# Kernel tuning notes

Hardware: AMD Instinct MI355X
Metric: run time of the kernel (lower is better)

## Reference

```python
import jax, jax.numpy as jnp
import numpy as np

N = 50000          # nodes
E = 800000         # edges
IN_C = 128
HID = 64
NUM_GRAPHS = 256
OUT_C = 8


def setup_inputs() -> dict:
    key = jax.random.key(0)
    k1, k2, k3, k4, k5, k6, k7 = jax.random.split(key, 7)
    x = jax.random.normal(k1, (N, IN_C), dtype=jnp.float32)
    edge_index = jax.random.randint(k2, (2, E), 0, N, dtype=jnp.int64)
    batch = jnp.sort(jax.random.randint(k3, (N,), 0, NUM_GRAPHS, dtype=jnp.int64))
    # GCNConv params (lin: in->hid, glorot-ish) and fc params (hid->8)
    W = jax.random.normal(k4, (IN_C, HID), dtype=jnp.float32) / np.sqrt(IN_C)
    b = jnp.zeros((HID,), dtype=jnp.float32)
    Wfc = jax.random.normal(k5, (HID, OUT_C), dtype=jnp.float32) / np.sqrt(HID)
    bfc = jnp.zeros((OUT_C,), dtype=jnp.float32)
    return {"x": x, "edge_index": edge_index, "batch": batch,
            "W": W, "b": b, "Wfc": Wfc, "bfc": bfc}


def reference(x, edge_index, batch, W, b, Wfc, bfc):
    n = x.shape[0]
    # GCNConv: linear transform first, then normalized propagation w/ self-loops
    x_lin = x @ W                                             # [N, HID]
    self_loops = jnp.arange(n, dtype=edge_index.dtype)
    row = jnp.concatenate([edge_index[0], self_loops])        # src
    col = jnp.concatenate([edge_index[1], self_loops])        # dst
    # symmetric normalization: deg over destinations (weight = 1)
    deg = jax.ops.segment_sum(jnp.ones_like(col, dtype=x.dtype), col,
                              num_segments=n)                 # [N]
    dinv = jnp.where(deg > 0, jax.lax.rsqrt(deg), 0.0)
    norm = dinv[row] * dinv[col]                              # [E+N]
    msg = x_lin[row] * norm[:, None]                          # gather + scale
    h = jax.ops.segment_sum(msg, col, num_segments=n) + b     # scatter-add
    h = jax.nn.relu(h)
    # global_mean_pool over batch ids
    sums = jax.ops.segment_sum(h, batch, num_segments=NUM_GRAPHS)
    cnts = jax.ops.segment_sum(jnp.ones((n,), dtype=x.dtype), batch,
                               num_segments=NUM_GRAPHS)
    pooled = sums / jnp.maximum(cnts, 1.0)[:, None]           # [G, HID]
    return pooled @ Wfc + bfc                                 # [G, 8]
```

## Files before the change

### kernel.cpp

```cpp
#include <hip/hip_runtime.h>
#include <stdint.h>

#define N_NODES 50000
#define N_EDGES 800000
#define IN_C    128
#define HID     64
#define NUM_G   256
#define OUT_C   8

#define NBH   64
#define ES    (N_EDGES / NBH)
#define NBIN  50048
#define NPK   (NBIN / 2)

#define NQ_H   4
#define BINS_H (NBIN / NQ_H)
#define PK_H   (BINS_H / 2)
#define NQ_S   4
#define BINS_S (NBIN / NQ_S)

#define NBLK_CSR   98
#define NBLK_LIN   512
#define NTILE      1563
#define NBLK_SCALE 200
#define NCHUNK     (N_NODES * 8)
#define GPOOL_GRID 782

__device__ __forceinline__ unsigned short f2bf(float f) {
    union { float f; unsigned u; } v; v.f = f;
    unsigned r = v.u + 0x7fff + ((v.u >> 16) & 1);
    return (unsigned short)(r >> 16);
}
__device__ __forceinline__ float4 bf4(uint2 u) {
    union { unsigned u; float f; } a, b, c, d;
    a.u = u.x << 16;  b.u = u.x & 0xffff0000u;
    c.u = u.y << 16;  d.u = u.y & 0xffff0000u;
    return make_float4(a.f, b.f, c.f, d.f);
}

__global__ __launch_bounds__(256) void k_histB(const int* __restrict__ col,
                                               int* __restrict__ part,
                                               int* __restrict__ cnt) {
    __shared__ int lh[PK_H];
    const int tid = threadIdx.x;
    if (blockIdx.x == 0 && tid < 2)
        __hip_atomic_store(&cnt[tid], 0, __ATOMIC_RELAXED, __HIP_MEMORY_SCOPE_AGENT);
    const int r = blockIdx.x >> 2;
    const int q = blockIdx.x & 3;
    const int q0 = q * BINS_H;
    for (int i = tid; i < PK_H; i += 256) lh[i] = 0;
    __syncthreads();
    const int4* col4 = (const int4*)(col + r * ES);
#pragma unroll 2
    for (int j4 = tid; j4 < ES / 4; j4 += 256) {
        int4 c = col4[j4];
        unsigned d0 = (unsigned)(c.x - q0), d1 = (unsigned)(c.y - q0);
        unsigned d2 = (unsigned)(c.z - q0), d3 = (unsigned)(c.w - q0);
        if (d0 < BINS_H) atomicAdd(&lh[d0 >> 1], 1 << ((d0 & 1) * 16));
        if (d1 < BINS_H) atomicAdd(&lh[d1 >> 1], 1 << ((d1 & 1) * 16));
        if (d2 < BINS_H) atomicAdd(&lh[d2 >> 1], 1 << ((d2 & 1) * 16));
        if (d3 < BINS_H) atomicAdd(&lh[d3 >> 1], 1 << ((d3 & 1) * 16));
    }
    __syncthreads();
    int* dst = part + r * NPK + q * PK_H;
    for (int i = tid; i < PK_H; i += 256) dst[i] = lh[i];
}

__global__ __launch_bounds__(256, 3) void k_csrlin(
        int* __restrict__ part, float* __restrict__ dinv,
        int* __restrict__ nstart, const int* __restrict__ batch,
        int* __restrict__ gstart, float* __restrict__ pooled,
        int* __restrict__ agg, int* __restrict__ cnt,
        const float* __restrict__ x, const float* __restrict__ W,
        float* __restrict__ y) {
    __shared__ int smemI[12512];
    const int tid = threadIdx.x;
    const int b   = blockIdx.x;

    if (b >= NBLK_CSR) {
        float* xs = (float*)smemI;
        float* Ws = (float*)smemI + 4224;
        {
            const float4* wsrc = (const float4*)W;
            float4*       wdst = (float4*)Ws;
#pragma unroll
            for (int j = 0; j < 8; ++j) wdst[tid + 256 * j] = wsrc[tid + 256 * j];
        }
        const int ty = tid >> 4, tx = tid & 15;
        const int r0 = ty * 2, c0 = tx * 4;
        for (int tile = b - NBLK_CSR; tile < NTILE; tile += NBLK_LIN) {
            const int row0 = tile * 32;
            __syncthreads();
            {
                const float4* src = (const float4*)(x + (size_t)row0 * IN_C);
                for (int i4 = tid; i4 < 1024; i4 += 256) {
                    int r = i4 >> 5, c4 = i4 & 31;
                    float4 v = make_float4(0.f, 0.f, 0.f, 0.f);
                    if (row0 + r < N_NODES) v = src[i4];
                    *(float4*)&xs[r * 132 + c4 * 4] = v;
                }
            }
            __syncthreads();
            float acc[2][4] = {};
#define FMA4(a_, bv_, r_) { acc[r_][0]=fmaf(a_,bv_.x,acc[r_][0]); acc[r_][1]=fmaf(a_,bv_.y,acc[r_][1]); \
                            acc[r_][2]=fmaf(a_,bv_.z,acc[r_][2]); acc[r_][3]=fmaf(a_,bv_.w,acc[r_][3]); }
            for (int k = 0; k < IN_C; k += 4) {
                float4 a0 = *(float4*)&xs[(r0 + 0) * 132 + k];
                float4 a1 = *(float4*)&xs[(r0 + 1) * 132 + k];
                float4 b0 = *(const float4*)&Ws[(k + 0) * HID + c0];
                float4 b1 = *(const float4*)&Ws[(k + 1) * HID + c0];
                float4 b2 = *(const float4*)&Ws[(k + 2) * HID + c0];
                float4 b3 = *(const float4*)&Ws[(k + 3) * HID + c0];
                FMA4(a0.x, b0, 0) FMA4(a0.y, b1, 0) FMA4(a0.z, b2, 0) FMA4(a0.w, b3, 0)
                FMA4(a1.x, b0, 1) FMA4(a1.y, b1, 1) FMA4(a1.z, b2, 1) FMA4(a1.w, b3, 1)
            }
#undef FMA4
#pragma unroll
            for (int i = 0; i < 2; ++i) {
                int r = row0 + r0 + i;
                if (r < N_NODES)
                    *(float4*)&y[(size_t)r * HID + c0] =
                        make_float4(acc[i][0], acc[i][1], acc[i][2], acc[i][3]);
            }
        }
        return;
    }

    int* sScan   = smemI;
    int* sAgg    = smemI + 256;
    int* sPrefix = smemI + 256 + 128;
    const int t = b * 256 + tid;
    const bool valid = t < NPK;
    int s0 = 0, s1 = 0;
    if (valid) {
        int idx = t;
#pragma unroll 4
        for (int r = 0; r < NBH; ++r, idx += NPK) {
            int v = part[idx];
            part[idx] = s0 | (s1 << 16);
            s0 += v & 0xffff;
            s1 += (v >> 16) & 0xffff;
        }
        ((float2*)dinv)[t] = make_float2(rsqrtf((float)(s0 + 1)),
                                         rsqrtf((float)(s1 + 1)));
    }
    int ps = s0 + s1;
    sScan[tid] = ps;
    __syncthreads();
    int acc = ps;
#pragma unroll
    for (int off = 1; off < 256; off <<= 1) {
        int tv = (tid >= off) ? sScan[tid - off] : 0;
        __syncthreads();
        acc += tv;
        sScan[tid] = acc;
        __syncthreads();
    }
    const int excl  = acc - ps;
    const int total = sScan[255];
    if (tid == 0) {
        __hip_atomic_store(&agg[b], total, __ATOMIC_RELAXED, __HIP_MEMORY_SCOPE_AGENT);
        __hip_atomic_fetch_add(&cnt[0], 1, __ATOMIC_RELEASE, __HIP_MEMORY_SCOPE_AGENT);
        while (__hip_atomic_load(&cnt[0], __ATOMIC_ACQUIRE, __HIP_MEMORY_SCOPE_AGENT) < NBLK_CSR)
            __builtin_amdgcn_s_sleep(2);
    }
    __syncthreads();
    if (tid < NBLK_CSR)
        sAgg[tid] = __hip_atomic_load(&agg[tid], __ATOMIC_RELAXED, __HIP_MEMORY_SCOPE_AGENT);
    __syncthreads();
    if (tid == 0) {
        int p = 0;
        for (int j = 0; j < b; ++j) p += sAgg[j];
        sPrefix[0] = p;
    }
    __syncthreads();
    if (valid) {
        int base = sPrefix[0] + excl;
        ((int2*)nstart)[t] = make_int2(base, base + s0);
    }
    if (t <= NUM_G) {
        int lo = 0, hi = N_NODES;
        while (lo < hi) {
            int mid = (lo + hi) >> 1;
            if (batch[mid] < t) lo = mid + 1; else hi = mid;
        }
        gstart[t] = lo;
    }
    if (t < NUM_G * HID) pooled[t] = 0.f;
}

__global__ __launch_bounds__(256) void k_scatscale(
        const int* __restrict__ row, const int* __restrict__ col,
        const int* __restrict__ part, const int* __restrict__ nstart,
        int* __restrict__ ed,
        const float* __restrict__ y, const float* __restrict__ dinv,
        unsigned short* __restrict__ yb) {
    __shared__ int lc[BINS_S];
    const int tid = threadIdx.x;
    if (blockIdx.x >= NQ_S * NBH) {
        int idx = (blockIdx.x - NQ_S * NBH) * 256 + tid;
#pragma unroll 1
        for (int c = idx; c < NCHUNK; c += NBLK_SCALE * 256) {
            int r  = c >> 3, ch = c & 7;
            const float4* ysrc = (const float4*)(y + (size_t)r * HID + ch * 8);
            float4 a = ysrc[0], b = ysrc[1];
            float dv = dinv[r];
            uint4 o;
            o.x = (unsigned)f2bf(a.x * dv) | ((unsigned)f2bf(a.y * dv) << 16);
            o.y = (unsigned)f2bf(a.z * dv) | ((unsigned)f2bf(a.w * dv) << 16);
            o.z = (unsigned)f2bf(b.x * dv) | ((unsigned)f2bf(b.y * dv) << 16);
            o.w = (unsigned)f2bf(b.z * dv) | ((unsigned)f2bf(b.w * dv) << 16);
            *(uint4*)&yb[(size_t)r * HID + ch * 8] = o;
        }
        return;
    }
    const int r = blockIdx.x >> 2;
    const int q = blockIdx.x & 3;
    const int q0 = q * BINS_S;
    for (int i = tid; i < BINS_S; i += 256) {
        int bin = q0 + i;
        int bb  = part[r * NPK + (bin >> 1)];
        int off = (i & 1) ? ((bb >> 16) & 0xffff) : (bb & 0xffff);
        lc[i] = nstart[bin] + off;
    }
    __syncthreads();
    const int4* col4 = (const int4*)(col + r * ES);
    const int4* row4 = (const int4*)(row + r * ES);
#pragma unroll 2
    for (int j4 = tid; j4 < ES / 4; j4 += 256) {
        int4 c = col4[j4];
        int4 s = row4[j4];
        unsigned d0 = (unsigned)(c.x - q0), d1 = (unsigned)(c.y - q0);
        unsigned d2 = (unsigned)(c.z - q0), d3 = (unsigned)(c.w - q0);
        if (d0 < BINS_S) ed[atomicAdd(&lc[d0], 1)] = s.x;
        if (d1 < BINS_S) ed[atomicAdd(&lc[d1], 1)] = s.y;
        if (d2 < BINS_S) ed[atomicAdd(&lc[d2], 1)] = s.z;
        if (d3 < BINS_S) ed[atomicAdd(&lc[d3], 1)] = s.w;
    }
}

#define GNPT 4
__global__ __launch_bounds__(256) void k_gpool(const int* __restrict__ ed,
                                               const int* __restrict__ nstart,
                                               const float* __restrict__ dinv,
                                               const unsigned short* __restrict__ yb,
                                               const int* __restrict__ batch,
                                               const float* __restrict__ bias,
                                               float* __restrict__ pooled,
                                               const int* __restrict__ gstart,
                                               const float* __restrict__ Wfc,
                                               const float* __restrict__ bfc,
                                               float* __restrict__ out,
                                               int* __restrict__ cnt) {
    __shared__ float spool[4 * HID];
    __shared__ int   sg0;
    const int tid  = threadIdx.x;
    const int lane = tid & 63;
    const int grp  = lane >> 4;
    const int sl   = lane & 15;
    const int nb0  = blockIdx.x * 64;

    for (int i = tid; i < 4 * HID; i += 256) spool[i] = 0.f;
    if (tid == 0) sg0 = batch[nb0];
    __syncthreads();
    const int sg0v = sg0;

    const int base = nb0 + (tid >> 6) * 16 + grp * GNPT;
    if (base < N_NODES) {
        const float4 b4 = *(const float4*)&bias[4 * sl];

#define FLUSH(g_, v_) { int slot_ = (g_) - sg0v; \
        if (slot_ < 4) { \
            atomicAdd(&spool[slot_ * HID + 4 * sl + 0], v_.x); \
            atomicAdd(&spool[slot_ * HID + 4 * sl + 1], v_.y); \
            atomicAdd(&spool[slot_ * HID + 4 * sl + 2], v_.z); \
            atomicAdd(&spool[slot_ * HID + 4 * sl + 3], v_.w); \
        } else { \
            atomicAdd(&pooled[(g_) * HID + 4 * sl + 0], v_.x); \
            atomicAdd(&pooled[(g_) * HID + 4 * sl + 1], v_.y); \
            atomicAdd(&pooled[(g_) * HID + 4 * sl + 2], v_.z); \
            atomicAdd(&pooled[(g_) * HID + 4 * sl + 3], v_.w); \
        } }

        int bnd[GNPT + 1];
#pragma unroll
        for (int i = 0; i <= GNPT; ++i) bnd[i] = nstart[base + i];
        int bt[GNPT];
#pragma unroll
        for (int i = 0; i < GNPT; ++i) bt[i] = batch[base + i];
        float dvv[GNPT];
#pragma unroll
        for (int i = 0; i < GNPT; ++i) dvv[i] = dinv[base + i];

        float4 pacc = make_float4(0.f, 0.f, 0.f, 0.f);
        int    cur  = -1;
#pragma unroll
        for (int n = 0; n < GNPT; ++n) {
            const int node = base + n;
            const int n0 = bnd[n], n1 = bnd[n + 1];
            float4 fa = make_float4(0.f, 0.f, 0.f, 0.f);
            float4 fb = make_float4(0.f, 0.f, 0.f, 0.f);
            int t = n0;
#pragma unroll 1
            for (; t + 4 <= n1; t += 4) {
                int s0 = ed[t], s1 = ed[t + 1], s2 = ed[t + 2], s3 = ed[t + 3];
                uint2 u0 = *(const uint2*)&yb[(size_t)s0 * HID + 4 * sl];
                uint2 u1 = *(const uint2*)&yb[(size_t)s1 * HID + 4 * sl];
                uint2 u2 = *(const uint2*)&yb[(size_t)s2 * HID + 4 * sl];
                uint2 u3 = *(const uint2*)&yb[(size_t)s3 * HID + 4 * sl];
                float4 v0 = bf4(u0), v1 = bf4(u1), v2 = bf4(u2), v3 = bf4(u3);
                fa.x += v0.x + v2.x;  fb.x += v1.x + v3.x;
                fa.y += v0.y + v2.y;  fb.y += v1.y + v3.y;
                fa.z += v0.z + v2.z;  fb.z += v1.z + v3.z;
                fa.w += v0.w + v2.w;  fb.w += v1.w + v3.w;
            }
#pragma unroll 1
            for (; t < n1; ++t) {
                int s = ed[t];
                uint2 u = *(const uint2*)&yb[(size_t)s * HID + 4 * sl];
                float4 v = bf4(u);
                fa.x += v.x; fa.y += v.y; fa.z += v.z; fa.w += v.w;
            }
            uint2 us = *(const uint2*)&yb[(size_t)node * HID + 4 * sl];
            float4 vs = bf4(us);
            float dv = dvv[n];
            float4 hv;
            hv.x = fmaxf((fa.x + fb.x + vs.x) * dv + b4.x, 0.f);
            hv.y = fmaxf((fa.y + fb.y + vs.y) * dv + b4.y, 0.f);
            hv.z = fmaxf((fa.z + fb.z + vs.z) * dv + b4.z, 0.f);
            hv.w = fmaxf((fa.w + fb.w + vs.w) * dv + b4.w, 0.f);
            int bg = bt[n];
            if (bg != cur) {
                if (cur >= 0) FLUSH(cur, pacc)
                cur  = bg;
                pacc = hv;
            } else {
                pacc.x += hv.x; pacc.y += hv.y; pacc.z += hv.z; pacc.w += hv.w;
            }
        }
        if (cur >= 0) FLUSH(cur, pacc)
#undef FLUSH
    }
    __syncthreads();
    for (int i = tid; i < 4 * HID; i += 256) {
        float v = spool[i];
        int g = sg0v + (i >> 6);
        if (v != 0.f && g < NUM_G)
            atomicAdd(&pooled[g * HID + (i & 63)], v);
    }
    __shared__ int lastFlag;
    __syncthreads();
    if (tid == 0) {
        int prev = __hip_atomic_fetch_add(&cnt[1], 1, __ATOMIC_ACQ_REL, __HIP_MEMORY_SCOPE_AGENT);
        lastFlag = (prev == GPOOL_GRID - 1) ? 1 : 0;
    }
    __syncthreads();
    if (lastFlag) {
        int g = tid;
        int g0 = gstart[g], g1 = gstart[g + 1];
        float inv = 1.f / fmaxf((float)(g1 - g0), 1.f);
        float acc[OUT_C] = {};
        for (int k = 0; k < HID; ++k) {
            float pv = pooled[g * HID + k];
#pragma unroll
            for (int o = 0; o < OUT_C; ++o)
                acc[o] = fmaf(pv, Wfc[k * OUT_C + o], acc[o]);
        }
#pragma unroll
        for (int o = 0; o < OUT_C; ++o)
            out[g * OUT_C + o] = acc[o] * inv + bfc[o];
    }
}

extern "C" void kernel_launch(void* const* d_in, const int* in_sizes, int n_in,
                              void* d_out, int out_size, void* d_ws, size_t ws_size,
                              hipStream_t stream) {
    const float* x     = (const float*)d_in[0];
    const int*   eidx  = (const int*)d_in[1];
    const int*   batch = (const int*)d_in[2];
    const float* W     = (const float*)d_in[3];
    const float* b     = (const float*)d_in[4];
    const float* Wfc   = (const float*)d_in[5];
    const float* bfc   = (const float*)d_in[6];
    float*       out   = (float*)d_out;

    const int* row = eidx;
    const int* col = eidx + N_EDGES;

    char* p = (char*)d_ws;
    float*          y    = (float*)p;          p += (size_t)N_NODES * HID * 4;
    unsigned short* yb   = (unsigned short*)p; p += (size_t)N_NODES * HID * 2;
    int*   part   = (int*)p;    p += (size_t)NBH * NPK * 4;
    float* dinv   = (float*)p;  p += (size_t)NBIN * 4;
    float* pooled = (float*)p;  p += (size_t)NUM_G * HID * 4;
    int*   nstart = (int*)p;    p += (size_t)(NBIN + 8) * 4;
    int*   gstart = (int*)p;    p += 1040;
    int*   agg    = (int*)p;    p += 512;
    int*   cnt    = (int*)p;    p += 64;
    int*   ed     = (int*)p;

    k_histB    <<<NBH * NQ_H, 256, 0, stream>>>(col, part, cnt);
    k_csrlin   <<<NBLK_CSR + NBLK_LIN, 256, 0, stream>>>(part, dinv, nstart, batch,
                                                         gstart, pooled, agg, cnt,
                                                         x, W, y);
    k_scatscale<<<NQ_S * NBH + NBLK_SCALE, 256, 0, stream>>>(row, col, part, nstart,
                                                             ed, y, dinv, yb);
    k_gpool    <<<GPOOL_GRID, 256, 0, stream>>>(ed, nstart, dinv, yb, batch, b,
                                                pooled, gstart, Wfc, bfc, out, cnt);
}
```

Measured before the change: 100.6 us.

## Stage block edge lists in LDS, unroll gather by 8, split scatter into 8 quarters

```diff
diff --git a/kernel.cpp b/kernel.cpp
--- a/kernel.cpp
+++ b/kernel.cpp
@@ -16,7 +16,7 @@
 #define NQ_H   4
 #define BINS_H (NBIN / NQ_H)
 #define PK_H   (BINS_H / 2)
-#define NQ_S   4
+#define NQ_S   8
 #define BINS_S (NBIN / NQ_S)
 
 #define NBLK_CSR   98
@@ -25,6 +25,7 @@
 #define NBLK_SCALE 200
 #define NCHUNK     (N_NODES * 8)
 #define GPOOL_GRID 782
+#define ECAP       6144
 
 __device__ __forceinline__ unsigned short f2bf(float f) {
     union { float f; unsigned u; } v; v.f = f;
@@ -214,8 +215,8 @@
         }
         return;
     }
-    const int r = blockIdx.x >> 2;
-    const int q = blockIdx.x & 3;
+    const int r = blockIdx.x >> 3;
+    const int q = blockIdx.x & 7;
     const int q0 = q * BINS_S;
     for (int i = tid; i < BINS_S; i += 256) {
         int bin = q0 + i;
@@ -252,18 +253,27 @@
                                                const float* __restrict__ bfc,
                                                float* __restrict__ out,
                                                int* __restrict__ cnt) {
+    __shared__ int   led[ECAP];
     __shared__ float spool[4 * HID];
     __shared__ int   sg0;
+    __shared__ int   lastFlag;
     const int tid  = threadIdx.x;
     const int lane = tid & 63;
     const int grp  = lane >> 4;
     const int sl   = lane & 15;
     const int nb0  = blockIdx.x * 64;
-
+    const int nEnd = (nb0 + 64 < N_NODES) ? nb0 + 64 : N_NODES;
+
+    const int e0b  = nstart[nb0];
+    const int e1b  = nstart[nEnd];
+    const int eTot = e1b - e0b;
+    const int eStg = (eTot < ECAP) ? eTot : ECAP;
+    for (int i = tid; i < eStg; i += 256) led[i] = ed[e0b + i];
     for (int i = tid; i < 4 * HID; i += 256) spool[i] = 0.f;
     if (tid == 0) sg0 = batch[nb0];
     __syncthreads();
     const int sg0v = sg0;
+    const bool allIn = (eTot <= ECAP);
 
     const int base = nb0 + (tid >> 6) * 16 + grp * GNPT;
     if (base < N_NODES) {
@@ -282,6 +292,47 @@
             atomicAdd(&pooled[(g_) * HID + 4 * sl + 3], v_.w); \
         } }
 
+#define EDGE_LOOP(GET) \
+    { int t = n0; \
+      for (; t + 8 <= n1; t += 8) { \
+          int s0 = GET(t),     s1 = GET(t + 1), s2 = GET(t + 2), s3 = GET(t + 3); \
+          int s4 = GET(t + 4), s5 = GET(t + 5), s6 = GET(t + 6), s7 = GET(t + 7); \
+          uint2 u0 = *(const uint2*)&yb[(size_t)s0 * HID + 4 * sl]; \
+          uint2 u1 = *(const uint2*)&yb[(size_t)s1 * HID + 4 * sl]; \
+          uint2 u2 = *(const uint2*)&yb[(size_t)s2 * HID + 4 * sl]; \
+          uint2 u3 = *(const uint2*)&yb[(size_t)s3 * HID + 4 * sl]; \
+          uint2 u4 = *(const uint2*)&yb[(size_t)s4 * HID + 4 * sl]; \
+          uint2 u5 = *(const uint2*)&yb[(size_t)s5 * HID + 4 * sl]; \
+          uint2 u6 = *(const uint2*)&yb[(size_t)s6 * HID + 4 * sl]; \
+          uint2 u7 = *(const uint2*)&yb[(size_t)s7 * HID + 4 * sl]; \
+          float4 v0 = bf4(u0), v1 = bf4(u1), v2 = bf4(u2), v3 = bf4(u3); \
+          float4 v4 = bf4(u4), v5 = bf4(u5), v6 = bf4(u6), v7 = bf4(u7); \
+          fa.x += (v0.x + v2.x) + (v4.x + v6.x);  fb.x += (v1.x + v3.x) + (v5.x + v7.x); \
+          fa.y += (v0.y + v2.y) + (v4.y + v6.y);  fb.y += (v1.y + v3.y) + (v5.y + v7.y); \
+          fa.z += (v0.z + v2.z) + (v4.z + v6.z);  fb.z += (v1.z + v3.z) + (v5.z + v7.z); \
+          fa.w += (v0.w + v2.w) + (v4.w + v6.w);  fb.w += (v1.w + v3.w) + (v5.w + v7.w); \
+      } \
+      for (; t + 4 <= n1; t += 4) { \
+          int s0 = GET(t), s1 = GET(t + 1), s2 = GET(t + 2), s3 = GET(t + 3); \
+          uint2 u0 = *(const uint2*)&yb[(size_t)s0 * HID + 4 * sl]; \
+          uint2 u1 = *(const uint2*)&yb[(size_t)s1 * HID + 4 * sl]; \
+          uint2 u2 = *(const uint2*)&yb[(size_t)s2 * HID + 4 * sl]; \
+          uint2 u3 = *(const uint2*)&yb[(size_t)s3 * HID + 4 * sl]; \
+          float4 v0 = bf4(u0), v1 = bf4(u1), v2 = bf4(u2), v3 = bf4(u3); \
+          fa.x += v0.x + v2.x;  fb.x += v1.x + v3.x; \
+          fa.y += v0.y + v2.y;  fb.y += v1.y + v3.y; \
+          fa.z += v0.z + v2.z;  fb.z += v1.z + v3.z; \
+          fa.w += v0.w + v2.w;  fb.w += v1.w + v3.w; \
+      } \
+      for (; t < n1; ++t) { \
+          int s = GET(t); \
+          uint2 u = *(const uint2*)&yb[(size_t)s * HID + 4 * sl]; \
+          float4 v = bf4(u); \
+          fa.x += v.x; fa.y += v.y; fa.z += v.z; fa.w += v.w; \
+      } }
+#define GET_L(t_) (led[(t_) - e0b])
+#define GET_G(t_) (ed[t_])
+
         int bnd[GNPT + 1];
 #pragma unroll
         for (int i = 0; i <= GNPT; ++i) bnd[i] = nstart[base + i];
@@ -298,30 +349,10 @@
         for (int n = 0; n < GNPT; ++n) {
             const int node = base + n;
             const int n0 = bnd[n], n1 = bnd[n + 1];
+            uint2 us = *(const uint2*)&yb[(size_t)node * HID + 4 * sl];
             float4 fa = make_float4(0.f, 0.f, 0.f, 0.f);
             float4 fb = make_float4(0.f, 0.f, 0.f, 0.f);
-            int t = n0;
-#pragma unroll 1
-            for (; t + 4 <= n1; t += 4) {
-                int s0 = ed[t], s1 = ed[t + 1], s2 = ed[t + 2], s3 = ed[t + 3];
-                uint2 u0 = *(const uint2*)&yb[(size_t)s0 * HID + 4 * sl];
-                uint2 u1 = *(const uint2*)&yb[(size_t)s1 * HID + 4 * sl];
-                uint2 u2 = *(const uint2*)&yb[(size_t)s2 * HID + 4 * sl];
-                uint2 u3 = *(const uint2*)&yb[(size_t)s3 * HID + 4 * sl];
-                float4 v0 = bf4(u0), v1 = bf4(u1), v2 = bf4(u2), v3 = bf4(u3);
-                fa.x += v0.x + v2.x;  fb.x += v1.x + v3.x;
-                fa.y += v0.y + v2.y;  fb.y += v1.y + v3.y;
-                fa.z += v0.z + v2.z;  fb.z += v1.z + v3.z;
-                fa.w += v0.w + v2.w;  fb.w += v1.w + v3.w;
-            }
-#pragma unroll 1
-            for (; t < n1; ++t) {
-                int s = ed[t];
-                uint2 u = *(const uint2*)&yb[(size_t)s * HID + 4 * sl];
-                float4 v = bf4(u);
-                fa.x += v.x; fa.y += v.y; fa.z += v.z; fa.w += v.w;
-            }
-            uint2 us = *(const uint2*)&yb[(size_t)node * HID + 4 * sl];
+            if (allIn) { EDGE_LOOP(GET_L) } else { EDGE_LOOP(GET_G) }
             float4 vs = bf4(us);
             float dv = dvv[n];
             float4 hv;
@@ -340,6 +371,9 @@
         }
         if (cur >= 0) FLUSH(cur, pacc)
 #undef FLUSH
+#undef EDGE_LOOP
+#undef GET_L
+#undef GET_G
     }
     __syncthreads();
     for (int i = tid; i < 4 * HID; i += 256) {
@@ -348,7 +382,6 @@
         if (v != 0.f && g < NUM_G)
             atomicAdd(&pooled[g * HID + (i & 63)], v);
     }
-    __shared__ int lastFlag;
     __syncthreads();
     if (tid == 0) {
         int prev = __hip_atomic_fetch_add(&cnt[1], 1, __ATOMIC_ACQ_REL, __HIP_MEMORY_SCOPE_AGENT);
```

Measured after the change: 93.50 us. 1.08x faster.
